# Kernel tuning notes

Hardware: AMD Instinct MI355X
Metric: run time of the kernel (lower is better)

## Reference

```python
import jax, jax.numpy as jnp
import numpy as np

H, DH, ITERS, EPS, LN_EPS = 8, 32, 3, 1e-8, 1e-5

def _ln(x, w, b):
    m = jnp.mean(x, axis=-1, keepdims=True)
    v = jnp.mean(jnp.square(x - m), axis=-1, keepdims=True)
    return (x - m) * jax.lax.rsqrt(v + LN_EPS) * w + b

def setup_inputs() -> dict:
    key = jax.random.key(0)
    ks = jax.random.split(key, 16)
    B, N, D, S = 64, 4096, 256, 8
    DI = H * DH  # 256
    HID = max(D, 128)
    s = 0.02
    return {
        "inputs": jax.random.normal(ks[0], (B, N, D), jnp.float32),
        "noise": jax.random.normal(ks[1], (B, S, D), jnp.float32),
        "slots_mean": jax.random.normal(ks[2], (1, 1, D), jnp.float32),
        "slots_logvar": jax.random.normal(ks[3], (1, 1, D), jnp.float32) * s,
        "wq": jax.random.normal(ks[4], (D, DI), jnp.float32) * s,
        "bq": jnp.zeros((DI,), jnp.float32),
        "wk": jax.random.normal(ks[5], (D, DI), jnp.float32) * s,
        "bk": jnp.zeros((DI,), jnp.float32),
        "wv": jax.random.normal(ks[6], (D, DI), jnp.float32) * s,
        "bv": jnp.zeros((DI,), jnp.float32),
        "wo": jax.random.normal(ks[7], (DI, D), jnp.float32) * s,
        "bo": jnp.zeros((D,), jnp.float32),
        "w_ih": jax.random.normal(ks[8], (D, 3 * D), jnp.float32) * s,
        "b_ih": jnp.zeros((3 * D,), jnp.float32),
        "w_hh": jax.random.normal(ks[9], (D, 3 * D), jnp.float32) * s,
        "b_hh": jnp.zeros((3 * D,), jnp.float32),
        "w1": jax.random.normal(ks[10], (D, HID), jnp.float32) * s,
        "b1": jnp.zeros((HID,), jnp.float32),
        "w2": jax.random.normal(ks[11], (HID, D), jnp.float32) * s,
        "b2": jnp.zeros((D,), jnp.float32),
        "ln_in_w": jnp.ones((D,), jnp.float32), "ln_in_b": jnp.zeros((D,), jnp.float32),
        "ln_s_w": jnp.ones((D,), jnp.float32), "ln_s_b": jnp.zeros((D,), jnp.float32),
        "ln_ff_w": jnp.ones((D,), jnp.float32), "ln_ff_b": jnp.zeros((D,), jnp.float32),
    }

def reference(inputs, noise, slots_mean, slots_logvar, wq, bq, wk, bk, wv, bv,
              wo, bo, w_ih, b_ih, w_hh, b_hh, w1, b1, w2, b2,
              ln_in_w, ln_in_b, ln_s_w, ln_s_b, ln_ff_w, ln_ff_b):
    B, N, D = inputs.shape
    S = noise.shape[1]
    scale = D ** -0.5  # note: scale uses dim, per original code
    # slot init: mean + exp(logvar) * noise (faithful: exp(logvar) used directly)
    slots = slots_mean + jnp.exp(slots_logvar) * noise  # [B,S,D]
    x = _ln(inputs, ln_in_w, ln_in_b)
    k = (x @ wk + bk).reshape(B, N, H, DH).transpose(0, 2, 1, 3)  # [B,H,N,Dh]
    v = (x @ wv + bv).reshape(B, N, H, DH).transpose(0, 2, 1, 3)
    attn = None
    for _ in range(ITERS):
        slots_prev = slots
        s = _ln(slots, ln_s_w, ln_s_b)
        q = (s @ wq + bq).reshape(B, S, H, DH).transpose(0, 2, 1, 3)  # [B,H,S,Dh]
        dots = jnp.einsum('bhid,bhjd->bhij', q, k) * scale  # [B,H,S,N]
        attn = jax.nn.softmax(dots, axis=-2)  # softmax over slot axis
        attn = attn + EPS
        attn = attn / jnp.clip(jnp.sum(attn, axis=-1, keepdims=True), 1e-12)  # L1 over inputs
        upd = jnp.einsum('bhjd,bhij->bhid', v, attn)  # [B,H,S,Dh]
        upd = upd.transpose(0, 2, 1, 3).reshape(B, S, H * DH) @ wo + bo  # [B,S,D]
        # GRUCell (torch gate order r,z,n)
        xg = upd.reshape(B * S, D) @ w_ih + b_ih
        hg = slots_prev.reshape(B * S, D) @ w_hh + b_hh
        xr, xz, xn = jnp.split(xg, 3, axis=-1)
        hr, hz, hn = jnp.split(hg, 3, axis=-1)
        r = jax.nn.sigmoid(xr + hr)
        z = jax.nn.sigmoid(xz + hz)
        n = jnp.tanh(xn + r * hn)
        slots = ((1.0 - z) * n + z * slots_prev.reshape(B * S, D)).reshape(B, S, D)
        ff = _ln(slots, ln_ff_w, ln_ff_b)
        slots = slots + (jax.nn.relu(ff @ w1 + b1) @ w2 + b2)
    return slots, attn
```

## Files before the change

kernel.cpp:

```cpp
#include <hip/hip_runtime.h>
#include <stdint.h>

typedef __attribute__((ext_vector_type(8))) short bf16x8;
typedef __attribute__((ext_vector_type(4))) float f32x4;

__device__ __forceinline__ float b2f(unsigned short s) {
    unsigned int u = ((unsigned int)s) << 16;
    return __builtin_bit_cast(float, u);
}
__device__ __forceinline__ unsigned short f2b(float f) {
    unsigned int u = __builtin_bit_cast(unsigned int, f);
    u += 0x7FFFu + ((u >> 16) & 1u);
    return (unsigned short)(u >> 16);
}

#define EPS_ATTN 1e-8f
#define LN_EPS 1e-5f
#define SCALE 0.0625f

__global__ __launch_bounds__(256) void k_prep(const float* __restrict__ wk,
                                              const float* __restrict__ wv,
                                              unsigned short* __restrict__ W3) {
    int g = blockIdx.x * 256 + threadIdx.x;
    int j = g & 7;
    int f = (g >> 3) & 1023;
    int stage = g >> 13;
    int p = f & 15, qq = (f >> 4) & 3, ntl = f >> 6;
    int kc = stage >> 1, half_ = stage & 1;
    int k = kc * 32 + qq * 8 + j;
    int n = half_ * 256 + ntl * 16 + p;
    float v = (n < 256) ? wk[k * 256 + n] : wv[k * 256 + (n - 256)];
    W3[g] = f2b(v);
}

__global__ __launch_bounds__(256) void k_init(const float* __restrict__ sm,
                                              const float* __restrict__ slv,
                                              const float* __restrict__ noise,
                                              float* __restrict__ slots) {
    int idx = blockIdx.x * 256 + threadIdx.x;
    int d = idx & 255;
    slots[idx] = sm[d] + expf(slv[d]) * noise[idx];
}

__global__ __launch_bounds__(256, 2) void k_kv(
    const float* __restrict__ x, const float* __restrict__ lnw, const float* __restrict__ lnb,
    const unsigned short* __restrict__ W3, const float* __restrict__ bk, const float* __restrict__ bv,
    unsigned short* __restrict__ Kb, unsigned short* __restrict__ Vb) {
    __shared__ __align__(16) unsigned short sh[16384];
    __shared__ __align__(16) float bL[512];
    unsigned short* As = sh;
    int t = threadIdx.x;
    int w = t >> 6, lane = t & 63;
    int p = lane & 15, q = lane >> 4;

    if (t < 128) {
        float4 bb = (t < 64) ? ((const float4*)bk)[t] : ((const float4*)bv)[t - 64];
        *(float4*)&bL[t * 4] = bb;
    }

    float4 lw  = ((const float4*)lnw)[lane];
    float4 lbv = ((const float4*)lnb)[lane];
    float4 xv[16];
    const float* xbase = x + ((size_t)blockIdx.x * 64 + w * 16) * 256;
    #pragma unroll
    for (int i = 0; i < 16; ++i) xv[i] = ((const float4*)(xbase + i * 256))[lane];
    int kcw = lane >> 3, qw = (lane >> 1) & 3, j0 = (lane & 1) * 4;
    #pragma unroll
    for (int i = 0; i < 16; ++i) {
        float4 v = xv[i];
        float s0 = v.x + v.y + v.z + v.w;
        float s1 = v.x * v.x + v.y * v.y + v.z * v.z + v.w * v.w;
        #pragma unroll
        for (int o = 1; o < 64; o <<= 1) { s0 += __shfl_xor(s0, o); s1 += __shfl_xor(s1, o); }
        float mean = s0 * (1.0f / 256.0f);
        float var  = s1 * (1.0f / 256.0f) - mean * mean;
        float rstd = rsqrtf(var + LN_EPS);
        ushort4 pk;
        pk.x = f2b((v.x - mean) * rstd * lw.x + lbv.x);
        pk.y = f2b((v.y - mean) * rstd * lw.y + lbv.y);
        pk.z = f2b((v.z - mean) * rstd * lw.z + lbv.z);
        pk.w = f2b((v.w - mean) * rstd * lw.w + lbv.w);
        int pos = (qw * 16 + i) ^ kcw;
        *(ushort4*)&As[((w * 8 + kcw) * 64 + pos) * 8 + j0] = pk;
    }
    __syncthreads();

    f32x4 acc[4][8];
    f32x4 zero = {0.f, 0.f, 0.f, 0.f};
    #pragma unroll
    for (int rt = 0; rt < 4; ++rt)
        #pragma unroll
        for (int ct = 0; ct < 8; ++ct) acc[rt][ct] = zero;

    const unsigned short* WbL = W3 + lane * 8;
    #pragma unroll 2
    for (int kc = 0; kc < 8; ++kc) {
        bf16x8 af[4];
        #pragma unroll
        for (int rt = 0; rt < 4; ++rt)
            af[rt] = *(const bf16x8*)&As[((rt * 8 + kc) * 64 + ((q * 16 + p) ^ kc)) * 8];
        #pragma unroll
        for (int ct = 0; ct < 8; ++ct) {
            int half_ = ct >> 2;
            int ntl = w * 4 + (ct & 3);
            bf16x8 bf = *(const bf16x8*)(WbL + (size_t)kc * 16384 + half_ * 8192 + ntl * 512);
            #pragma unroll
            for (int rt = 0; rt < 4; ++rt)
                acc[rt][ct] = __builtin_amdgcn_mfma_f32_16x16x32_bf16(af[rt], bf, acc[rt][ct], 0, 0, 0);
        }
    }
    __syncthreads();

    unsigned short* rep = As;
    int b_  = blockIdx.x >> 6;
    int n0g = (blockIdx.x & 63) * 64;

    #pragma unroll
    for (int ct = 0; ct < 4; ++ct) {
        int col = w * 64 + ct * 16 + p;
        float bias = bL[col];
        int hl = col >> 5, dh = col & 31;
        int dlo = dh & 7, dch = dh >> 3;
        int dchs = dch ^ q;
        #pragma unroll
        for (int rt = 0; rt < 4; ++rt) {
            #pragma unroll
            for (int r = 0; r < 4; ++r) {
                int nl = rt * 16 + q * 4 + r;
                rep[(hl * 64 + nl) * 32 + dchs * 8 + dlo] = f2b(acc[rt][ct][r] + bias);
            }
        }
    }
    __syncthreads();
    {
        int nl = t >> 2, dhc = t & 3;
        int swz = (nl >> 2) & 3;
        #pragma unroll
        for (int i = 0; i < 8; ++i) {
            uint4 vd = *(const uint4*)&rep[((i * 64 + nl) * 32) + ((dhc ^ swz) * 8)];
            *(uint4*)(Kb + (((size_t)b_ * 8 + i) * 4096 + n0g + nl) * 32 + dhc * 8) = vd;
        }
    }
    __syncthreads();

    #pragma unroll
    for (int ct = 4; ct < 8; ++ct) {
        int vrow = w * 64 + (ct - 4) * 16 + p;
        float bias = bL[256 + vrow];
        #pragma unroll
        for (int rt = 0; rt < 4; ++rt) {
            int chunk = (rt * 4 + q) ^ (p & 14);
            ushort4 pk;
            pk.x = f2b(acc[rt][ct][0] + bias);
            pk.y = f2b(acc[rt][ct][1] + bias);
            pk.z = f2b(acc[rt][ct][2] + bias);
            pk.w = f2b(acc[rt][ct][3] + bias);
            *(ushort4*)&rep[vrow * 64 + chunk * 4] = pk;
        }
    }
    __syncthreads();
    #pragma unroll
    for (int i = 0; i < 8; ++i) {
        int vrow = i * 32 + (t >> 3);
        int c16 = t & 7;
        uint4 vd = *(const uint4*)&rep[vrow * 64 + ((2 * c16) ^ (vrow & 14)) * 4];
        *(uint4*)(Vb + ((size_t)(b_ * 8 + (vrow >> 5)) * 32 + (vrow & 31)) * 4096 + n0g + c16 * 8) = vd;
    }
}

__global__ __launch_bounds__(256) void k_q(
    const float* __restrict__ slots, const float* __restrict__ lnw, const float* __restrict__ lnb,
    const float* __restrict__ wq, const float* __restrict__ bq, float* __restrict__ qg) {
    __shared__ float sln[256];
    __shared__ float red[8];
    int t = threadIdx.x;
    int row = blockIdx.x;
    float v = slots[(size_t)row * 256 + t];
    float s0 = v, s1 = v * v;
    #pragma unroll
    for (int off = 1; off < 64; off <<= 1) { s0 += __shfl_xor(s0, off); s1 += __shfl_xor(s1, off); }
    if ((t & 63) == 0) { red[t >> 6] = s0; red[4 + (t >> 6)] = s1; }
    __syncthreads();
    float ts0 = red[0] + red[1] + red[2] + red[3];
    float ts1 = red[4] + red[5] + red[6] + red[7];
    float mean = ts0 * (1.f / 256.f);
    float var  = ts1 * (1.f / 256.f) - mean * mean;
    float rstd = rsqrtf(var + LN_EPS);
    sln[t] = (v - mean) * rstd * lnw[t] + lnb[t];
    __syncthreads();
    float acc = bq[t];
    #pragma unroll 4
    for (int k = 0; k < 256; ++k) acc += sln[k] * wq[k * 256 + t];
    int b = row >> 3, sl = row & 7;
    qg[(size_t)b * 2048 + (t >> 5) * 256 + sl * 32 + (t & 31)] = acc;
}

__global__ __launch_bounds__(256) void k_pre(
    const unsigned short* __restrict__ Kg, const float* __restrict__ qg,
    float* __restrict__ rowsum_part) {
    __shared__ float srs[4][8];
    int t = threadIdx.x;
    int w = t >> 6, lane = t & 63;
    int c = lane & 15, g = lane >> 4;
    int bh = blockIdx.x >> 2;
    int chunk = blockIdx.x & 3;
    const unsigned short* Kbh = Kg + (size_t)bh * 4096 * 32;

    bf16x8 qhi = {0,0,0,0,0,0,0,0};
    bf16x8 qlo = {0,0,0,0,0,0,0,0};
    if (c < 8) {
        const float* qp = qg + (size_t)bh * 256 + c * 32 + g * 8;
        #pragma unroll
        for (int j = 0; j < 8; ++j) {
            float qv = qp[j];
            unsigned short hb = f2b(qv);
            qhi[j] = (short)hb;
            qlo[j] = (short)f2b(qv - b2f(hb));
        }
    }

    f32x4 zero = {0.f, 0.f, 0.f, 0.f};
    float rs = 0.f;
    int nb0 = chunk * 1024 + w * 256;

    #pragma unroll 2
    for (int pr = 0; pr < 8; ++pr) {
        int base = nb0 + pr * 32;
        bf16x8 k0 = *(const bf16x8*)(Kbh + (size_t)(base + c) * 32 + g * 8);
        bf16x8 k1 = *(const bf16x8*)(Kbh + (size_t)(base + 16 + c) * 32 + g * 8);
        f32x4 s0 = __builtin_amdgcn_mfma_f32_16x16x32_bf16(k0, qhi, zero, 0, 0, 0);
        s0 = __builtin_amdgcn_mfma_f32_16x16x32_bf16(k0, qlo, s0, 0, 0, 0);
        f32x4 s1 = __builtin_amdgcn_mfma_f32_16x16x32_bf16(k1, qhi, zero, 0, 0, 0);
        s1 = __builtin_amdgcn_mfma_f32_16x16x32_bf16(k1, qlo, s1, 0, 0, 0);
        float d0[4], d1[4];
        #pragma unroll
        for (int r = 0; r < 4; ++r) { d0[r] = s0[r] * SCALE; d1[r] = s1[r] * SCALE; }
        float m = fmaxf(fmaxf(fmaxf(d0[0], d0[1]), fmaxf(d0[2], d0[3])),
                        fmaxf(fmaxf(d1[0], d1[1]), fmaxf(d1[2], d1[3])));
        m = fmaxf(m, __shfl_xor(m, 1));
        m = fmaxf(m, __shfl_xor(m, 2));
        m = fmaxf(m, __shfl_xor(m, 4));
        m = fmaxf(m, __shfl_xor(m, 8));
        #pragma unroll
        for (int r = 0; r < 4; ++r) {
            float e0 = __expf(d0[r] - m);
            float e1 = __expf(d1[r] - m);
            float t0 = e0;
            t0 += __shfl_xor(t0, 1); t0 += __shfl_xor(t0, 2); t0 += __shfl_xor(t0, 4);
            float t1 = e1;
            t1 += __shfl_xor(t1, 1); t1 += __shfl_xor(t1, 2); t1 += __shfl_xor(t1, 4);
            rs += (e0 * (1.0f / t0) + EPS_ATTN) + (e1 * (1.0f / t1) + EPS_ATTN);
        }
    }
    rs += __shfl_xor(rs, 16);
    rs += __shfl_xor(rs, 32);
    if (lane < 8) srs[w][lane] = rs;
    __syncthreads();
    if (t < 8) {
        rowsum_part[((size_t)bh * 4 + chunk) * 8 + t] =
            srs[0][t] + srs[1][t] + srs[2][t] + srs[3][t];
    }
}

__global__ __launch_bounds__(256) void k_attn(
    const unsigned short* __restrict__ Kg, const unsigned short* __restrict__ VTg,
    const float* __restrict__ qg, float* __restrict__ upd_part, float* __restrict__ rowsum_part,
    float* __restrict__ attn_out, int last) {
    __shared__ float supd[4][256];
    __shared__ float srs[4][8];
    int t = threadIdx.x;
    int w = t >> 6, lane = t & 63;
    int c = lane & 15;
    int g = lane >> 4;

    int bh = blockIdx.x >> 2;
    int chunk = blockIdx.x & 3;
    const unsigned short* Kbh = Kg  + (size_t)bh * 4096 * 32;
    const unsigned short* Vbh = VTg + (size_t)bh * 32 * 4096;

    bf16x8 qhi = {0,0,0,0,0,0,0,0};
    bf16x8 qlo = {0,0,0,0,0,0,0,0};
    if (c < 8) {
        const float* qp = qg + (size_t)bh * 256 + c * 32 + g * 8;
        #pragma unroll
        for (int j = 0; j < 8; ++j) {
            float qv = qp[j];
            unsigned short hb = f2b(qv);
            qhi[j] = (short)hb;
            qlo[j] = (short)f2b(qv - b2f(hb));
        }
    }
    float ainv = 0.f;
    if (last && c < 8) {
        float rsum = 0.f;
        #pragma unroll
        for (int ch = 0; ch < 4; ++ch) rsum += rowsum_part[((size_t)bh * 4 + ch) * 8 + c];
        ainv = 1.0f / fmaxf(rsum, 1e-12f);
    }

    f32x4 zero = {0.f, 0.f, 0.f, 0.f};
    f32x4 accL = zero, accH = zero;
    float rs = 0.f;
    int nb0 = chunk * 1024 + w * 256;

    #pragma unroll 2
    for (int pr = 0; pr < 8; ++pr) {
        int base = nb0 + pr * 32;
        bf16x8 k0 = *(const bf16x8*)(Kbh + (size_t)(base + c) * 32 + g * 8);
        bf16x8 k1 = *(const bf16x8*)(Kbh + (size_t)(base + 16 + c) * 32 + g * 8);
        const unsigned short* vlo = Vbh + (size_t)c * 4096 + base + g * 4;
        const unsigned short* vhi = Vbh + (size_t)(c + 16) * 4096 + base + g * 4;
        union { ushort4 h[2]; bf16x8 v; } V0, V1;
        V0.h[0] = *(const ushort4*)vlo;
        V0.h[1] = *(const ushort4*)(vlo + 16);
        V1.h[0] = *(const ushort4*)vhi;
        V1.h[1] = *(const ushort4*)(vhi + 16);

        f32x4 s0 = __builtin_amdgcn_mfma_f32_16x16x32_bf16(k0, qhi, zero, 0, 0, 0);
        s0 = __builtin_amdgcn_mfma_f32_16x16x32_bf16(k0, qlo, s0, 0, 0, 0);
        f32x4 s1 = __builtin_amdgcn_mfma_f32_16x16x32_bf16(k1, qhi, zero, 0, 0, 0);
        s1 = __builtin_amdgcn_mfma_f32_16x16x32_bf16(k1, qlo, s1, 0, 0, 0);

        float d0[4], d1[4];
        #pragma unroll
        for (int r = 0; r < 4; ++r) { d0[r] = s0[r] * SCALE; d1[r] = s1[r] * SCALE; }
        float m = fmaxf(fmaxf(fmaxf(d0[0], d0[1]), fmaxf(d0[2], d0[3])),
                        fmaxf(fmaxf(d1[0], d1[1]), fmaxf(d1[2], d1[3])));
        m = fmaxf(m, __shfl_xor(m, 1));
        m = fmaxf(m, __shfl_xor(m, 2));
        m = fmaxf(m, __shfl_xor(m, 4));
        m = fmaxf(m, __shfl_xor(m, 8));
        float a0[4], a1[4];
        #pragma unroll
        for (int r = 0; r < 4; ++r) {
            float e0 = __expf(d0[r] - m);
            float e1 = __expf(d1[r] - m);
            float t0 = e0;
            t0 += __shfl_xor(t0, 1); t0 += __shfl_xor(t0, 2); t0 += __shfl_xor(t0, 4);
            float t1 = e1;
            t1 += __shfl_xor(t1, 1); t1 += __shfl_xor(t1, 2); t1 += __shfl_xor(t1, 4);
            a0[r] = e0 * (1.0f / t0) + EPS_ATTN;
            a1[r] = e1 * (1.0f / t1) + EPS_ATTN;
            rs += a0[r] + a1[r];
        }
        if (last && c < 8) {
            float4 st0 = {a0[0] * ainv, a0[1] * ainv, a0[2] * ainv, a0[3] * ainv};
            float4 st1 = {a1[0] * ainv, a1[1] * ainv, a1[2] * ainv, a1[3] * ainv};
            float* ap = attn_out + ((size_t)bh * 8 + c) * 4096 + base + g * 4;
            *(float4*)ap = st0;
            *(float4*)(ap + 16) = st1;
        }
        bf16x8 pah, pal;
        float af[8] = {a0[0], a0[1], a0[2], a0[3], a1[0], a1[1], a1[2], a1[3]};
        #pragma unroll
        for (int j = 0; j < 8; ++j) {
            unsigned short hb = f2b(af[j]);
            pah[j] = (short)hb;
            pal[j] = (short)f2b(af[j] - b2f(hb));
        }
        accL = __builtin_amdgcn_mfma_f32_16x16x32_bf16(V0.v, pah, accL, 0, 0, 0);
        accL = __builtin_amdgcn_mfma_f32_16x16x32_bf16(V0.v, pal, accL, 0, 0, 0);
        accH = __builtin_amdgcn_mfma_f32_16x16x32_bf16(V1.v, pah, accH, 0, 0, 0);
        accH = __builtin_amdgcn_mfma_f32_16x16x32_bf16(V1.v, pal, accH, 0, 0, 0);
    }

    if (!last) {
        rs += __shfl_xor(rs, 16);
        rs += __shfl_xor(rs, 32);
        if (lane < 8) srs[w][lane] = rs;
    }
    if (c < 8) {
        float* up = &supd[w][c * 32 + g * 4];
        up[0]  = accL[0]; up[1]  = accL[1]; up[2]  = accL[2]; up[3]  = accL[3];
        up[16] = accH[0]; up[17] = accH[1]; up[18] = accH[2]; up[19] = accH[3];
    }
    __syncthreads();
    {
        float v = supd[0][t] + supd[1][t] + supd[2][t] + supd[3][t];
        upd_part[((size_t)bh * 4 + chunk) * 256 + t] = v;
    }
    if (!last && t < 8) {
        float v = srs[0][t] + srs[1][t] + srs[2][t] + srs[3][t];
        rowsum_part[((size_t)bh * 4 + chunk) * 8 + t] = v;
    }
}

__global__ __launch_bounds__(256) void k_gA(
    const float* __restrict__ upd_part, const float* __restrict__ rowsum_part,
    const float* __restrict__ wo, const float* __restrict__ bo,
    float* __restrict__ O) {
    __shared__ float Ul[8][256];
    __shared__ float Pp[4][8][64];
    int t = threadIdx.x;
    int b = blockIdx.x >> 2, cc = blockIdx.x & 3;
    int colbase = cc * 64;
    {
        int r = t >> 5, d0 = (t & 31) * 8;
        int h = (t & 31) >> 2;
        float rsum = 0.f;
        #pragma unroll
        for (int ch = 0; ch < 4; ++ch)
            rsum += rowsum_part[((size_t)(b * 8 + h) * 4 + ch) * 8 + r];
        float inv = 1.0f / fmaxf(rsum, 1e-12f);
        float u[8] = {0.f,0.f,0.f,0.f,0.f,0.f,0.f,0.f};
        #pragma unroll
        for (int ch = 0; ch < 4; ++ch) {
            const float* up = upd_part + ((size_t)(b * 8 + h) * 4 + ch) * 256 + r * 32 + (d0 & 31);
            float4 u0 = *(const float4*)up;
            float4 u1 = *(const float4*)(up + 4);
            u[0] += u0.x; u[1] += u0.y; u[2] += u0.z; u[3] += u0.w;
            u[4] += u1.x; u[5] += u1.y; u[6] += u1.z; u[7] += u1.w;
        }
        #pragma unroll
        for (int i = 0; i < 8; ++i) Ul[r][d0 + i] = u[i] * inv;
    }
    __syncthreads();
    int c = t & 63, kq = t >> 6;
    float acc[8] = {0.f,0.f,0.f,0.f,0.f,0.f,0.f,0.f};
    const float* wp = wo + (size_t)(kq * 64) * 256 + colbase + c;
    #pragma unroll 16
    for (int k = 0; k < 64; ++k) {
        float wv_ = wp[(size_t)k * 256];
        int kk = kq * 64 + k;
        #pragma unroll
        for (int r = 0; r < 8; ++r) acc[r] += Ul[r][kk] * wv_;
    }
    #pragma unroll
    for (int r = 0; r < 8; ++r) Pp[kq][r][c] = acc[r];
    __syncthreads();
    #pragma unroll
    for (int j = 0; j < 2; ++j) {
        int o = t * 2 + j;
        int r = o >> 6, c2 = o & 63;
        float v = Pp[0][r][c2] + Pp[1][r][c2] + Pp[2][r][c2] + Pp[3][r][c2] + bo[colbase + c2];
        O[(size_t)(b * 8 + r) * 256 + colbase + c2] = v;
    }
}

__global__ __launch_bounds__(256) void k_gB(
    const float* __restrict__ O, const float* __restrict__ slin,
    const float* __restrict__ wih, const float* __restrict__ bih,
    const float* __restrict__ whh, const float* __restrict__ bhh,
    float* __restrict__ gcomb, float* __restrict__ xn, float* __restrict__ hn) {
    __shared__ float Ol[8][256], Hl[8][256];
    __shared__ float Px[2][8][128], Ph[2][8][128];
    int t = threadIdx.x;
    int b = blockIdx.x / 6, cc = blockIdx.x % 6;
    int colbase = cc * 128;
    {
        int r = t >> 5, d0 = (t & 31) * 8;
        const float* op = O + (size_t)(b * 8 + r) * 256 + d0;
        const float* hp = slin + (size_t)(b * 8 + r) * 256 + d0;
        *(float4*)&Ol[r][d0]     = *(const float4*)op;
        *(float4*)&Ol[r][d0 + 4] = *(const float4*)(op + 4);
        *(float4*)&Hl[r][d0]     = *(const float4*)hp;
        *(float4*)&Hl[r][d0 + 4] = *(const float4*)(hp + 4);
    }
    __syncthreads();
    int c = t & 127, kh = t >> 7;
    float ax[8] = {0.f,0.f,0.f,0.f,0.f,0.f,0.f,0.f};
    float ah[8] = {0.f,0.f,0.f,0.f,0.f,0.f,0.f,0.f};
    const float* wxp = wih + (size_t)(kh * 128) * 768 + colbase + c;
    const float* whp = whh + (size_t)(kh * 128) * 768 + colbase + c;
    #pragma unroll 8
    for (int k = 0; k < 128; ++k) {
        float wx = wxp[(size_t)k * 768];
        float wh = whp[(size_t)k * 768];
        int kk = kh * 128 + k;
        #pragma unroll
        for (int r = 0; r < 8; ++r) { ax[r] += Ol[r][kk] * wx; ah[r] += Hl[r][kk] * wh; }
    }
    #pragma unroll
    for (int r = 0; r < 8; ++r) { Px[kh][r][c] = ax[r]; Ph[kh][r][c] = ah[r]; }
    __syncthreads();
    #pragma unroll
    for (int j = 0; j < 4; ++j) {
        int o = t * 4 + j;
        int r = o >> 7, c2 = o & 127;
        int cg = colbase + c2;
        int row = b * 8 + r;
        float vx = Px[0][r][c2] + Px[1][r][c2] + bih[cg];
        float vh = Ph[0][r][c2] + Ph[1][r][c2] + bhh[cg];
        if (cg < 512) {
            gcomb[(size_t)row * 512 + cg] = vx + vh;
        } else {
            xn[(size_t)row * 256 + cg - 512] = vx;
            hn[(size_t)row * 256 + cg - 512] = vh;
        }
    }
}

__global__ __launch_bounds__(256) void k_gC(
    const float* __restrict__ gcomb, const float* __restrict__ xn, const float* __restrict__ hn,
    const float* __restrict__ slin, const float* __restrict__ lnfw, const float* __restrict__ lnfb,
    float* __restrict__ slout, float* __restrict__ F) {
    __shared__ float red[8];
    int t = threadIdx.x, row = blockIdx.x;
    float a_r = gcomb[(size_t)row * 512 + t];
    float a_z = gcomb[(size_t)row * 512 + 256 + t];
    float xnv = xn[(size_t)row * 256 + t];
    float hnv = hn[(size_t)row * 256 + t];
    float hp  = slin[(size_t)row * 256 + t];
    float rg = 1.f / (1.f + expf(-a_r));
    float zg = 1.f / (1.f + expf(-a_z));
    float ng = tanhf(xnv + rg * hnv);
    float s1 = (1.f - zg) * ng + zg * hp;
    slout[(size_t)row * 256 + t] = s1;
    float s0 = s1, sq = s1 * s1;
    #pragma unroll
    for (int o = 1; o < 64; o <<= 1) { s0 += __shfl_xor(s0, o); sq += __shfl_xor(sq, o); }
    if ((t & 63) == 0) { red[t >> 6] = s0; red[4 + (t >> 6)] = sq; }
    __syncthreads();
    float ts0 = red[0] + red[1] + red[2] + red[3];
    float ts1 = red[4] + red[5] + red[6] + red[7];
    float mean = ts0 * (1.f / 256.f);
    float var  = ts1 * (1.f / 256.f) - mean * mean;
    float rstd = rsqrtf(var + LN_EPS);
    F[(size_t)row * 256 + t] = (s1 - mean) * rstd * lnfw[t] + lnfb[t];
}

__global__ __launch_bounds__(256) void k_gD(
    const float* __restrict__ F, const float* __restrict__ w1, const float* __restrict__ b1,
    float* __restrict__ H1) {
    __shared__ float Fl[8][256];
    __shared__ float Pp[4][8][64];
    int t = threadIdx.x;
    int b = blockIdx.x >> 2, cc = blockIdx.x & 3;
    int colbase = cc * 64;
    {
        int r = t >> 5, d0 = (t & 31) * 8;
        const float* fp = F + (size_t)(b * 8 + r) * 256 + d0;
        *(float4*)&Fl[r][d0]     = *(const float4*)fp;
        *(float4*)&Fl[r][d0 + 4] = *(const float4*)(fp + 4);
    }
    __syncthreads();
    int c = t & 63, kq = t >> 6;
    float acc[8] = {0.f,0.f,0.f,0.f,0.f,0.f,0.f,0.f};
    const float* wp = w1 + (size_t)(kq * 64) * 256 + colbase + c;
    #pragma unroll 16
    for (int k = 0; k < 64; ++k) {
        float wv_ = wp[(size_t)k * 256];
        int kk = kq * 64 + k;
        #pragma unroll
        for (int r = 0; r < 8; ++r) acc[r] += Fl[r][kk] * wv_;
    }
    #pragma unroll
    for (int r = 0; r < 8; ++r) Pp[kq][r][c] = acc[r];
    __syncthreads();
    #pragma unroll
    for (int j = 0; j < 2; ++j) {
        int o = t * 2 + j;
        int r = o >> 6, c2 = o & 63;
        float v = Pp[0][r][c2] + Pp[1][r][c2] + Pp[2][r][c2] + Pp[3][r][c2] + b1[colbase + c2];
        H1[(size_t)(b * 8 + r) * 256 + colbase + c2] = fmaxf(v, 0.f);
    }
}

__global__ __launch_bounds__(256) void k_gE(
    const float* __restrict__ H1, const float* __restrict__ w2, const float* __restrict__ b2,
    float* __restrict__ slout) {
    __shared__ float Hl[8][256];
    __shared__ float Pp[4][8][64];
    int t = threadIdx.x;
    int b = blockIdx.x >> 2, cc = blockIdx.x & 3;
    int colbase = cc * 64;
    {
        int r = t >> 5, d0 = (t & 31) * 8;
        const float* hp = H1 + (size_t)(b * 8 + r) * 256 + d0;
        *(float4*)&Hl[r][d0]     = *(const float4*)hp;
        *(float4*)&Hl[r][d0 + 4] = *(const float4*)(hp + 4);
    }
    __syncthreads();
    int c = t & 63, kq = t >> 6;
    float acc[8] = {0.f,0.f,0.f,0.f,0.f,0.f,0.f,0.f};
    const float* wp = w2 + (size_t)(kq * 64) * 256 + colbase + c;
    #pragma unroll 16
    for (int k = 0; k < 64; ++k) {
        float wv_ = wp[(size_t)k * 256];
        int kk = kq * 64 + k;
        #pragma unroll
        for (int r = 0; r < 8; ++r) acc[r] += Hl[r][kk] * wv_;
    }
    #pragma unroll
    for (int r = 0; r < 8; ++r) Pp[kq][r][c] = acc[r];
    __syncthreads();
    #pragma unroll
    for (int j = 0; j < 2; ++j) {
        int o = t * 2 + j;
        int r = o >> 6, c2 = o & 63;
        size_t idx = (size_t)(b * 8 + r) * 256 + colbase + c2;
        float v = Pp[0][r][c2] + Pp[1][r][c2] + Pp[2][r][c2] + Pp[3][r][c2] + b2[colbase + c2];
        slout[idx] = slout[idx] + v;
    }
}

extern "C" void kernel_launch(void* const* d_in, const int* in_sizes, int n_in,
                              void* d_out, int out_size, void* d_ws, size_t ws_size,
                              hipStream_t stream) {
    const float* inputs = (const float*)d_in[0];
    const float* noise  = (const float*)d_in[1];
    const float* sm     = (const float*)d_in[2];
    const float* slv    = (const float*)d_in[3];
    const float* wq     = (const float*)d_in[4];
    const float* bq     = (const float*)d_in[5];
    const float* wk     = (const float*)d_in[6];
    const float* bk     = (const float*)d_in[7];
    const float* wv     = (const float*)d_in[8];
    const float* bv     = (const float*)d_in[9];
    const float* wo     = (const float*)d_in[10];
    const float* bo     = (const float*)d_in[11];
    const float* wih    = (const float*)d_in[12];
    const float* bih    = (const float*)d_in[13];
    const float* whh    = (const float*)d_in[14];
    const float* bhh    = (const float*)d_in[15];
    const float* w1     = (const float*)d_in[16];
    const float* b1     = (const float*)d_in[17];
    const float* w2     = (const float*)d_in[18];
    const float* b2     = (const float*)d_in[19];
    const float* lniw   = (const float*)d_in[20];
    const float* lnib   = (const float*)d_in[21];
    const float* lnsw   = (const float*)d_in[22];
    const float* lnsb   = (const float*)d_in[23];
    const float* lnfw   = (const float*)d_in[24];
    const float* lnfb   = (const float*)d_in[25];

    char* ws = (char*)d_ws;
    unsigned short* Kb = (unsigned short*)ws;
    unsigned short* Vb = (unsigned short*)(ws + 134217728ull);
    float* slotsA  = (float*)(ws + 268435456ull);
    float* slotsB  = (float*)(ws + 268959744ull);
    float* Rr      = (float*)(ws + 269484032ull);
    float* Pr      = (float*)(ws + 270008320ull);
    float* Qr      = (float*)(ws + 270532608ull);
    float* rowsum_part = (float*)(ws + 272629760ull);
    unsigned short* W3 = (unsigned short*)Pr;
    float* O_  = Pr;
    float* upd_part = Qr;
    float* gcomb = Qr;
    float* xn = Qr + 262144;
    float* hn = Qr + 393216;
    float* H1 = Qr;
    float* qg = Rr;
    float* F_ = Rr;

    float* out_slots = (float*)d_out;
    float* attn_out  = (float*)d_out + 131072;

    k_prep<<<512, 256, 0, stream>>>(wk, wv, W3);
    k_init<<<512, 256, 0, stream>>>(sm, slv, noise, slotsA);
    k_kv<<<4096, 256, 0, stream>>>(inputs, lniw, lnib, W3, bk, bv, Kb, Vb);
    for (int it = 0; it < 3; ++it) {
        int last = (it == 2);
        float* sl_in  = (it == 0) ? slotsA : ((it == 1) ? slotsB : slotsA);
        float* sl_out = (it == 0) ? slotsB : ((it == 1) ? slotsA : out_slots);
        k_q<<<512, 256, 0, stream>>>(sl_in, lnsw, lnsb, wq, bq, qg);
        if (last) k_pre<<<2048, 256, 0, stream>>>(Kb, qg, rowsum_part);
        k_attn<<<2048, 256, 0, stream>>>(Kb, Vb, qg, upd_part, rowsum_part, attn_out, last);
        k_gA<<<256, 256, 0, stream>>>(upd_part, rowsum_part, wo, bo, O_);
        k_gB<<<384, 256, 0, stream>>>(O_, sl_in, wih, bih, whh, bhh, gcomb, xn, hn);
        k_gC<<<512, 256, 0, stream>>>(gcomb, xn, hn, sl_in, lnfw, lnfb, sl_out, F_);
        k_gD<<<256, 256, 0, stream>>>(F_, w1, b1, H1);
        k_gE<<<256, 256, 0, stream>>>(H1, w2, b2, sl_out);
    }
}
```

Before: 1.025 ms.

## Fuse slot update chain and next-iteration query projection into one kernel

Replaces the five per-iteration slot-update kernels (output projection, GRU gate GEMMs, GRU combine with LayerNorm, MLP layer 1, MLP layer 2) with a single kernel that handles two slot rows per block and keeps all intermediates in shared memory. For all but the last iteration it also computes the next iteration's LayerNorm and query projection, so the separate query kernel now runs only once before the loop. This removes several launches and global round-trips of intermediates. In exchange each block re-reads full weight matrices for only two rows, so weight traffic from cache grows, and only 256 blocks run.

After: 1.008 ms. No clear change (-1.6%).

```diff
diff --git a/kernel.cpp b/kernel.cpp
--- a/kernel.cpp
+++ b/kernel.cpp
@@ -385,212 +385,176 @@
     }
 }
 
-__global__ __launch_bounds__(256) void k_gA(
+__global__ __launch_bounds__(256) void k_upd(
     const float* __restrict__ upd_part, const float* __restrict__ rowsum_part,
+    const float* __restrict__ slin,
     const float* __restrict__ wo, const float* __restrict__ bo,
-    float* __restrict__ O) {
-    __shared__ float Ul[8][256];
-    __shared__ float Pp[4][8][64];
-    int t = threadIdx.x;
-    int b = blockIdx.x >> 2, cc = blockIdx.x & 3;
-    int colbase = cc * 64;
-    {
-        int r = t >> 5, d0 = (t & 31) * 8;
-        int h = (t & 31) >> 2;
-        float rsum = 0.f;
-        #pragma unroll
-        for (int ch = 0; ch < 4; ++ch)
-            rsum += rowsum_part[((size_t)(b * 8 + h) * 4 + ch) * 8 + r];
-        float inv = 1.0f / fmaxf(rsum, 1e-12f);
-        float u[8] = {0.f,0.f,0.f,0.f,0.f,0.f,0.f,0.f};
-        #pragma unroll
-        for (int ch = 0; ch < 4; ++ch) {
-            const float* up = upd_part + ((size_t)(b * 8 + h) * 4 + ch) * 256 + r * 32 + (d0 & 31);
-            float4 u0 = *(const float4*)up;
-            float4 u1 = *(const float4*)(up + 4);
-            u[0] += u0.x; u[1] += u0.y; u[2] += u0.z; u[3] += u0.w;
-            u[4] += u1.x; u[5] += u1.y; u[6] += u1.z; u[7] += u1.w;
-        }
-        #pragma unroll
-        for (int i = 0; i < 8; ++i) Ul[r][d0 + i] = u[i] * inv;
-    }
-    __syncthreads();
-    int c = t & 63, kq = t >> 6;
-    float acc[8] = {0.f,0.f,0.f,0.f,0.f,0.f,0.f,0.f};
-    const float* wp = wo + (size_t)(kq * 64) * 256 + colbase + c;
-    #pragma unroll 16
-    for (int k = 0; k < 64; ++k) {
-        float wv_ = wp[(size_t)k * 256];
-        int kk = kq * 64 + k;
-        #pragma unroll
-        for (int r = 0; r < 8; ++r) acc[r] += Ul[r][kk] * wv_;
-    }
-    #pragma unroll
-    for (int r = 0; r < 8; ++r) Pp[kq][r][c] = acc[r];
-    __syncthreads();
-    #pragma unroll
-    for (int j = 0; j < 2; ++j) {
-        int o = t * 2 + j;
-        int r = o >> 6, c2 = o & 63;
-        float v = Pp[0][r][c2] + Pp[1][r][c2] + Pp[2][r][c2] + Pp[3][r][c2] + bo[colbase + c2];
-        O[(size_t)(b * 8 + r) * 256 + colbase + c2] = v;
-    }
-}
-
-__global__ __launch_bounds__(256) void k_gB(
-    const float* __restrict__ O, const float* __restrict__ slin,
     const float* __restrict__ wih, const float* __restrict__ bih,
     const float* __restrict__ whh, const float* __restrict__ bhh,
-    float* __restrict__ gcomb, float* __restrict__ xn, float* __restrict__ hn) {
-    __shared__ float Ol[8][256], Hl[8][256];
-    __shared__ float Px[2][8][128], Ph[2][8][128];
+    const float* __restrict__ lnfw, const float* __restrict__ lnfb,
+    const float* __restrict__ w1, const float* __restrict__ b1,
+    const float* __restrict__ w2, const float* __restrict__ b2,
+    const float* __restrict__ lnsw, const float* __restrict__ lnsb,
+    const float* __restrict__ wq, const float* __restrict__ bq,
+    float* __restrict__ slout, float* __restrict__ qg, int do_q) {
+    __shared__ float Ul[2][256];
+    __shared__ float Ol[2][256];
+    __shared__ float Hl[2][256];
+    __shared__ float Fl[2][256];
+    __shared__ float Xl[2][256];
+    __shared__ float red4[4][4];
     int t = threadIdx.x;
-    int b = blockIdx.x / 6, cc = blockIdx.x % 6;
-    int colbase = cc * 128;
-    {
-        int r = t >> 5, d0 = (t & 31) * 8;
-        const float* op = O + (size_t)(b * 8 + r) * 256 + d0;
-        const float* hp = slin + (size_t)(b * 8 + r) * 256 + d0;
-        *(float4*)&Ol[r][d0]     = *(const float4*)op;
-        *(float4*)&Ol[r][d0 + 4] = *(const float4*)(op + 4);
-        *(float4*)&Hl[r][d0]     = *(const float4*)hp;
-        *(float4*)&Hl[r][d0 + 4] = *(const float4*)(hp + 4);
-    }
-    __syncthreads();
-    int c = t & 127, kh = t >> 7;
-    float ax[8] = {0.f,0.f,0.f,0.f,0.f,0.f,0.f,0.f};
-    float ah[8] = {0.f,0.f,0.f,0.f,0.f,0.f,0.f,0.f};
-    const float* wxp = wih + (size_t)(kh * 128) * 768 + colbase + c;
-    const float* whp = whh + (size_t)(kh * 128) * 768 + colbase + c;
-    #pragma unroll 8
-    for (int k = 0; k < 128; ++k) {
-        float wx = wxp[(size_t)k * 768];
-        float wh = whp[(size_t)k * 768];
-        int kk = kh * 128 + k;
-        #pragma unroll
-        for (int r = 0; r < 8; ++r) { ax[r] += Ol[r][kk] * wx; ah[r] += Hl[r][kk] * wh; }
-    }
-    #pragma unroll
-    for (int r = 0; r < 8; ++r) { Px[kh][r][c] = ax[r]; Ph[kh][r][c] = ah[r]; }
-    __syncthreads();
-    #pragma unroll
-    for (int j = 0; j < 4; ++j) {
-        int o = t * 4 + j;
-        int r = o >> 7, c2 = o & 127;
-        int cg = colbase + c2;
-        int row = b * 8 + r;
-        float vx = Px[0][r][c2] + Px[1][r][c2] + bih[cg];
-        float vh = Ph[0][r][c2] + Ph[1][r][c2] + bhh[cg];
-        if (cg < 512) {
-            gcomb[(size_t)row * 512 + cg] = vx + vh;
-        } else {
-            xn[(size_t)row * 256 + cg - 512] = vx;
-            hn[(size_t)row * 256 + cg - 512] = vh;
-        }
-    }
-}
-
-__global__ __launch_bounds__(256) void k_gC(
-    const float* __restrict__ gcomb, const float* __restrict__ xn, const float* __restrict__ hn,
-    const float* __restrict__ slin, const float* __restrict__ lnfw, const float* __restrict__ lnfb,
-    float* __restrict__ slout, float* __restrict__ F) {
-    __shared__ float red[8];
-    int t = threadIdx.x, row = blockIdx.x;
-    float a_r = gcomb[(size_t)row * 512 + t];
-    float a_z = gcomb[(size_t)row * 512 + 256 + t];
-    float xnv = xn[(size_t)row * 256 + t];
-    float hnv = hn[(size_t)row * 256 + t];
-    float hp  = slin[(size_t)row * 256 + t];
-    float rg = 1.f / (1.f + expf(-a_r));
-    float zg = 1.f / (1.f + expf(-a_z));
-    float ng = tanhf(xnv + rg * hnv);
-    float s1 = (1.f - zg) * ng + zg * hp;
-    slout[(size_t)row * 256 + t] = s1;
-    float s0 = s1, sq = s1 * s1;
-    #pragma unroll
-    for (int o = 1; o < 64; o <<= 1) { s0 += __shfl_xor(s0, o); sq += __shfl_xor(sq, o); }
-    if ((t & 63) == 0) { red[t >> 6] = s0; red[4 + (t >> 6)] = sq; }
-    __syncthreads();
-    float ts0 = red[0] + red[1] + red[2] + red[3];
-    float ts1 = red[4] + red[5] + red[6] + red[7];
-    float mean = ts0 * (1.f / 256.f);
-    float var  = ts1 * (1.f / 256.f) - mean * mean;
-    float rstd = rsqrtf(var + LN_EPS);
-    F[(size_t)row * 256 + t] = (s1 - mean) * rstd * lnfw[t] + lnfb[t];
-}
-
-__global__ __launch_bounds__(256) void k_gD(
-    const float* __restrict__ F, const float* __restrict__ w1, const float* __restrict__ b1,
-    float* __restrict__ H1) {
-    __shared__ float Fl[8][256];
-    __shared__ float Pp[4][8][64];
-    int t = threadIdx.x;
-    int b = blockIdx.x >> 2, cc = blockIdx.x & 3;
-    int colbase = cc * 64;
-    {
-        int r = t >> 5, d0 = (t & 31) * 8;
-        const float* fp = F + (size_t)(b * 8 + r) * 256 + d0;
-        *(float4*)&Fl[r][d0]     = *(const float4*)fp;
-        *(float4*)&Fl[r][d0 + 4] = *(const float4*)(fp + 4);
-    }
-    __syncthreads();
-    int c = t & 63, kq = t >> 6;
-    float acc[8] = {0.f,0.f,0.f,0.f,0.f,0.f,0.f,0.f};
-    const float* wp = w1 + (size_t)(kq * 64) * 256 + colbase + c;
-    #pragma unroll 16
-    for (int k = 0; k < 64; ++k) {
-        float wv_ = wp[(size_t)k * 256];
-        int kk = kq * 64 + k;
-        #pragma unroll
-        for (int r = 0; r < 8; ++r) acc[r] += Fl[r][kk] * wv_;
-    }
-    #pragma unroll
-    for (int r = 0; r < 8; ++r) Pp[kq][r][c] = acc[r];
-    __syncthreads();
-    #pragma unroll
-    for (int j = 0; j < 2; ++j) {
-        int o = t * 2 + j;
-        int r = o >> 6, c2 = o & 63;
-        float v = Pp[0][r][c2] + Pp[1][r][c2] + Pp[2][r][c2] + Pp[3][r][c2] + b1[colbase + c2];
-        H1[(size_t)(b * 8 + r) * 256 + colbase + c2] = fmaxf(v, 0.f);
-    }
-}
-
-__global__ __launch_bounds__(256) void k_gE(
-    const float* __restrict__ H1, const float* __restrict__ w2, const float* __restrict__ b2,
-    float* __restrict__ slout) {
-    __shared__ float Hl[8][256];
-    __shared__ float Pp[4][8][64];
-    int t = threadIdx.x;
-    int b = blockIdx.x >> 2, cc = blockIdx.x & 3;
-    int colbase = cc * 64;
-    {
-        int r = t >> 5, d0 = (t & 31) * 8;
-        const float* hp = H1 + (size_t)(b * 8 + r) * 256 + d0;
-        *(float4*)&Hl[r][d0]     = *(const float4*)hp;
-        *(float4*)&Hl[r][d0 + 4] = *(const float4*)(hp + 4);
-    }
-    __syncthreads();
-    int c = t & 63, kq = t >> 6;
-    float acc[8] = {0.f,0.f,0.f,0.f,0.f,0.f,0.f,0.f};
-    const float* wp = w2 + (size_t)(kq * 64) * 256 + colbase + c;
-    #pragma unroll 16
-    for (int k = 0; k < 64; ++k) {
-        float wv_ = wp[(size_t)k * 256];
-        int kk = kq * 64 + k;
-        #pragma unroll
-        for (int r = 0; r < 8; ++r) acc[r] += Hl[r][kk] * wv_;
-    }
-    #pragma unroll
-    for (int r = 0; r < 8; ++r) Pp[kq][r][c] = acc[r];
-    __syncthreads();
-    #pragma unroll
-    for (int j = 0; j < 2; ++j) {
-        int o = t * 2 + j;
-        int r = o >> 6, c2 = o & 63;
-        size_t idx = (size_t)(b * 8 + r) * 256 + colbase + c2;
-        float v = Pp[0][r][c2] + Pp[1][r][c2] + Pp[2][r][c2] + Pp[3][r][c2] + b2[colbase + c2];
-        slout[idx] = slout[idx] + v;
+    int lane = t & 63, wvi = t >> 6;
+    int b = blockIdx.x >> 2, sp = blockIdx.x & 3;
+    int row0 = b * 8 + sp * 2;
+    int h = t >> 5, dd = t & 31;
+
+    #pragma unroll
+    for (int r = 0; r < 2; ++r) {
+        int sl = sp * 2 + r;
+        float rsum = 0.f, u = 0.f;
+        #pragma unroll
+        for (int ch = 0; ch < 4; ++ch) {
+            rsum += rowsum_part[((size_t)(b * 8 + h) * 4 + ch) * 8 + sl];
+            u    += upd_part[((size_t)(b * 8 + h) * 4 + ch) * 256 + sl * 32 + dd];
+        }
+        Ul[r][t] = u / fmaxf(rsum, 1e-12f);
+        Hl[r][t] = slin[(size_t)(row0 + r) * 256 + t];
+    }
+    __syncthreads();
+
+    {
+        float a0 = 0.f, a1 = 0.f;
+        #pragma unroll 8
+        for (int k = 0; k < 256; ++k) {
+            float w_ = wo[k * 256 + t];
+            a0 += Ul[0][k] * w_;
+            a1 += Ul[1][k] * w_;
+        }
+        float bb = bo[t];
+        Ol[0][t] = a0 + bb;
+        Ol[1][t] = a1 + bb;
+    }
+    __syncthreads();
+
+    float xg00 = 0.f, xg01 = 0.f, xg02 = 0.f, xg10 = 0.f, xg11 = 0.f, xg12 = 0.f;
+    float hg00 = 0.f, hg01 = 0.f, hg02 = 0.f, hg10 = 0.f, hg11 = 0.f, hg12 = 0.f;
+    #pragma unroll 4
+    for (int k = 0; k < 256; ++k) {
+        float o0 = Ol[0][k], o1 = Ol[1][k];
+        float p0 = Hl[0][k], p1 = Hl[1][k];
+        const float* wx = wih + (size_t)k * 768 + t;
+        const float* wh = whh + (size_t)k * 768 + t;
+        float wx0 = wx[0], wx1 = wx[256], wx2 = wx[512];
+        float wh0 = wh[0], wh1 = wh[256], wh2 = wh[512];
+        xg00 += o0 * wx0; xg01 += o0 * wx1; xg02 += o0 * wx2;
+        xg10 += o1 * wx0; xg11 += o1 * wx1; xg12 += o1 * wx2;
+        hg00 += p0 * wh0; hg01 += p0 * wh1; hg02 += p0 * wh2;
+        hg10 += p1 * wh0; hg11 += p1 * wh1; hg12 += p1 * wh2;
+    }
+    float bi0 = bih[t], bi1 = bih[256 + t], bi2 = bih[512 + t];
+    float bh0 = bhh[t], bh1 = bhh[256 + t], bh2 = bhh[512 + t];
+    float s1v0, s1v1;
+    {
+        float rg = 1.f / (1.f + expf(-((xg00 + bi0) + (hg00 + bh0))));
+        float zg = 1.f / (1.f + expf(-((xg01 + bi1) + (hg01 + bh1))));
+        float ng = tanhf((xg02 + bi2) + rg * (hg02 + bh2));
+        s1v0 = (1.f - zg) * ng + zg * Hl[0][t];
+        rg = 1.f / (1.f + expf(-((xg10 + bi0) + (hg10 + bh0))));
+        zg = 1.f / (1.f + expf(-((xg11 + bi1) + (hg11 + bh1))));
+        ng = tanhf((xg12 + bi2) + rg * (hg12 + bh2));
+        s1v1 = (1.f - zg) * ng + zg * Hl[1][t];
+    }
+
+    {
+        float a = s1v0, sa = s1v0 * s1v0, c = s1v1, sc = s1v1 * s1v1;
+        #pragma unroll
+        for (int o = 1; o < 64; o <<= 1) {
+            a += __shfl_xor(a, o); sa += __shfl_xor(sa, o);
+            c += __shfl_xor(c, o); sc += __shfl_xor(sc, o);
+        }
+        if (lane == 0) { red4[wvi][0] = a; red4[wvi][1] = sa; red4[wvi][2] = c; red4[wvi][3] = sc; }
+        __syncthreads();
+        float t0 = red4[0][0] + red4[1][0] + red4[2][0] + red4[3][0];
+        float t1 = red4[0][1] + red4[1][1] + red4[2][1] + red4[3][1];
+        float t2 = red4[0][2] + red4[1][2] + red4[2][2] + red4[3][2];
+        float t3 = red4[0][3] + red4[1][3] + red4[2][3] + red4[3][3];
+        float m0 = t0 * (1.f / 256.f), v0 = t1 * (1.f / 256.f) - m0 * m0;
+        float m1 = t2 * (1.f / 256.f), v1 = t3 * (1.f / 256.f) - m1 * m1;
+        float r0 = rsqrtf(v0 + LN_EPS), r1 = rsqrtf(v1 + LN_EPS);
+        float lw = lnfw[t], lb = lnfb[t];
+        Fl[0][t] = (s1v0 - m0) * r0 * lw + lb;
+        Fl[1][t] = (s1v1 - m1) * r1 * lw + lb;
+    }
+    __syncthreads();
+
+    {
+        float a0 = 0.f, a1 = 0.f;
+        #pragma unroll 8
+        for (int k = 0; k < 256; ++k) {
+            float w_ = w1[k * 256 + t];
+            a0 += Fl[0][k] * w_;
+            a1 += Fl[1][k] * w_;
+        }
+        float bb = b1[t];
+        Xl[0][t] = fmaxf(a0 + bb, 0.f);
+        Xl[1][t] = fmaxf(a1 + bb, 0.f);
+    }
+    __syncthreads();
+
+    float out0, out1;
+    {
+        float a0 = 0.f, a1 = 0.f;
+        #pragma unroll 8
+        for (int k = 0; k < 256; ++k) {
+            float w_ = w2[k * 256 + t];
+            a0 += Xl[0][k] * w_;
+            a1 += Xl[1][k] * w_;
+        }
+        float bb = b2[t];
+        out0 = s1v0 + a0 + bb;
+        out1 = s1v1 + a1 + bb;
+        slout[(size_t)(row0 + 0) * 256 + t] = out0;
+        slout[(size_t)(row0 + 1) * 256 + t] = out1;
+    }
+
+    if (!do_q) return;
+
+    __syncthreads();
+    {
+        float a = out0, sa = out0 * out0, c = out1, sc = out1 * out1;
+        #pragma unroll
+        for (int o = 1; o < 64; o <<= 1) {
+            a += __shfl_xor(a, o); sa += __shfl_xor(sa, o);
+            c += __shfl_xor(c, o); sc += __shfl_xor(sc, o);
+        }
+        if (lane == 0) { red4[wvi][0] = a; red4[wvi][1] = sa; red4[wvi][2] = c; red4[wvi][3] = sc; }
+        __syncthreads();
+        float t0 = red4[0][0] + red4[1][0] + red4[2][0] + red4[3][0];
+        float t1 = red4[0][1] + red4[1][1] + red4[2][1] + red4[3][1];
+        float t2 = red4[0][2] + red4[1][2] + red4[2][2] + red4[3][2];
+        float t3 = red4[0][3] + red4[1][3] + red4[2][3] + red4[3][3];
+        float m0 = t0 * (1.f / 256.f), v0 = t1 * (1.f / 256.f) - m0 * m0;
+        float m1 = t2 * (1.f / 256.f), v1 = t3 * (1.f / 256.f) - m1 * m1;
+        float r0 = rsqrtf(v0 + LN_EPS), r1 = rsqrtf(v1 + LN_EPS);
+        float lw = lnsw[t], lb = lnsb[t];
+        Xl[0][t] = (out0 - m0) * r0 * lw + lb;
+        Xl[1][t] = (out1 - m1) * r1 * lw + lb;
+    }
+    __syncthreads();
+    {
+        float a0 = 0.f, a1 = 0.f;
+        #pragma unroll 8
+        for (int k = 0; k < 256; ++k) {
+            float w_ = wq[k * 256 + t];
+            a0 += Xl[0][k] * w_;
+            a1 += Xl[1][k] * w_;
+        }
+        float bb = bq[t];
+        int sl0 = sp * 2;
+        int d5 = t >> 5, d31 = t & 31;
+        qg[(size_t)b * 2048 + d5 * 256 + sl0 * 32 + d31] = a0 + bb;
+        qg[(size_t)b * 2048 + d5 * 256 + (sl0 + 1) * 32 + d31] = a1 + bb;
     }
 }
 
@@ -634,14 +598,8 @@
     float* Qr      = (float*)(ws + 270532608ull);
     float* rowsum_part = (float*)(ws + 272629760ull);
     unsigned short* W3 = (unsigned short*)Pr;
-    float* O_  = Pr;
     float* upd_part = Qr;
-    float* gcomb = Qr;
-    float* xn = Qr + 262144;
-    float* hn = Qr + 393216;
-    float* H1 = Qr;
     float* qg = Rr;
-    float* F_ = Rr;
 
     float* out_slots = (float*)d_out;
     float* attn_out  = (float*)d_out + 131072;
@@ -649,17 +607,16 @@
     k_prep<<<512, 256, 0, stream>>>(wk, wv, W3);
     k_init<<<512, 256, 0, stream>>>(sm, slv, noise, slotsA);
     k_kv<<<4096, 256, 0, stream>>>(inputs, lniw, lnib, W3, bk, bv, Kb, Vb);
+    k_q<<<512, 256, 0, stream>>>(slotsA, lnsw, lnsb, wq, bq, qg);
     for (int it = 0; it < 3; ++it) {
         int last = (it == 2);
         float* sl_in  = (it == 0) ? slotsA : ((it == 1) ? slotsB : slotsA);
         float* sl_out = (it == 0) ? slotsB : ((it == 1) ? slotsA : out_slots);
-        k_q<<<512, 256, 0, stream>>>(sl_in, lnsw, lnsb, wq, bq, qg);
         if (last) k_pre<<<2048, 256, 0, stream>>>(Kb, qg, rowsum_part);
         k_attn<<<2048, 256, 0, stream>>>(Kb, Vb, qg, upd_part, rowsum_part, attn_out, last);
-        k_gA<<<256, 256, 0, stream>>>(upd_part, rowsum_part, wo, bo, O_);
-        k_gB<<<384, 256, 0, stream>>>(O_, sl_in, wih, bih, whh, bhh, gcomb, xn, hn);
-        k_gC<<<512, 256, 0, stream>>>(gcomb, xn, hn, sl_in, lnfw, lnfb, sl_out, F_);
-        k_gD<<<256, 256, 0, stream>>>(F_, w1, b1, H1);
-        k_gE<<<256, 256, 0, stream>>>(H1, w2, b2, sl_out);
-    }
-}
+        k_upd<<<256, 256, 0, stream>>>(upd_part, rowsum_part, sl_in,
+                                       wo, bo, wih, bih, whh, bhh, lnfw, lnfb,
+                                       w1, b1, w2, b2, lnsw, lnsb, wq, bq,
+                                       sl_out, qg, last ? 0 : 1);
+    }
+}
```
